# Optimization experiments

Hardware: AMD Instinct MI355X
Metric: run time of the kernel (lower is better)

## Reference

```python
import jax, jax.numpy as jnp
import numpy as np

H = 64; H2 = 32; B = 256; NPART = 64
NP = B * NPART          # 16384 part nodes
PER_TF = 512            # torque/force nodes per graph
NT = B * PER_TF; NF = NT
E = 262144              # edges per edge type
L = 5; T = 4            # 4 main hetero layers + 1 actor layer; 4 edge types
NEG = 0.2; EPS = 1e-5


def _seg_softmax(e, seg, n):
    # softmax over entries sharing the same segment id (along axis 0)
    m = jax.lax.stop_gradient(jax.ops.segment_max(e, seg, num_segments=n))
    ex = jnp.exp(e - m[seg])
    s = jax.ops.segment_sum(ex, seg, num_segments=n)
    return ex / s[seg]


def _gat(x_s, x_d, es, ed, Ws, Wd, a_s, a_d, b, n_dst):
    # PyG GATConv, heads=1, add_self_loops=False, bipartite (x_src, x_dst)
    hs = x_s @ Ws                      # [Ns,H]
    hd = x_d @ Wd                      # [Nd,H]
    e = jax.nn.leaky_relu((hs @ a_s)[es] + (hd @ a_d)[ed], NEG)   # [E]
    al = _seg_softmax(e, ed, n_dst)                                # attn per dst neighborhood
    return jax.ops.segment_sum(al[:, None] * hs[es], ed, num_segments=n_dst) + b


def _hetero_layer(xp, xt, xf, edges, Ws, Wd, a_s, a_d, b):
    # to_hetero(aggr='sum'): one GATConv per edge type, sum into each dst type
    (pts, ptd), (tps, tpd), (pfs, pfd), (fps, fpd) = edges
    out_t = _gat(xp, xt, pts, ptd, Ws[0], Wd[0], a_s[0], a_d[0], b[0], xt.shape[0])
    out_p = (_gat(xt, xp, tps, tpd, Ws[1], Wd[1], a_s[1], a_d[1], b[1], xp.shape[0])
             + _gat(xf, xp, fps, fpd, Ws[3], Wd[3], a_s[3], a_d[3], b[3], xp.shape[0]))
    out_f = _gat(xp, xf, pfs, pfd, Ws[2], Wd[2], a_s[2], a_d[2], b[2], xf.shape[0])
    return out_p, out_t, out_f


def _pool(x):
    # MultiAggregation([max, min, mean]); segments are uniform -> reshape
    xr = x.reshape(B, -1, x.shape[-1])
    return jnp.concatenate([xr.max(1), xr.min(1), xr.mean(1)], axis=-1)


def reference(mass, part_state, torque_x, force_x,
              e_pt_src, e_pt_dst, e_tp_src, e_tp_dst,
              e_pf_src, e_pf_dst, e_fp_src, e_fp_dst,
              batch, part_id,
              emb_parts_W, emb_state, W_src, W_dst, a_src, a_dst, b_conv,
              ln_gamma, ln_beta, out_a_W, out_a_b,
              innet_W, innet_b, full_W, full_b, outnet_W, outnet_b):
    edges = ((e_pt_src, e_pt_dst), (e_tp_src, e_tp_dst),
             (e_pf_src, e_pf_dst), (e_fp_src, e_fp_dst))
    idx = part_state[:, 0] + 2 * part_state[:, 1]
    xp = jnp.concatenate([mass @ emb_parts_W, emb_state[idx]], axis=-1)  # [NP,H]
    xt, xf = torque_x, force_x
    for l in range(4):  # main hetero GAT, ReLU between layers, none after last
        xp, xt, xf = _hetero_layer(xp, xt, xf, edges,
                                   W_src[l], W_dst[l], a_src[l], a_dst[l], b_conv[l])
        if l < 3:
            xp, xt, xf = jax.nn.relu(xp), jax.nn.relu(xt), jax.nn.relu(xf)
    # actor: 1-layer hetero GAT (no activation)
    ap, at, af = _hetero_layer(xp, xt, xf, edges,
                               W_src[4], W_dst[4], a_src[4], a_dst[4], b_conv[4])
    # node LayerNorm
    mu = ap.mean(-1, keepdims=True)
    var = ((ap - mu) ** 2).mean(-1, keepdims=True)
    ra = (ap - mu) / jnp.sqrt(var + EPS) * ln_gamma + ln_beta
    ra = ra @ out_a_W + out_a_b                         # [NP,2]
    soft = _seg_softmax(ra, batch, B)                   # softmax per graph, per channel
    actions = jnp.zeros((B, 2, NPART), dtype=ra.dtype).at[batch, :, part_id].set(soft)
    actions = actions.reshape(B, 2 * NPART)
    rep = jnp.concatenate([_pool(xp), _pool(xt), _pool(xf)], axis=1)   # [B, 9H]
    repV = jax.nn.gelu(rep @ innet_W + innet_b, approximate=False)
    repV = jax.nn.gelu(repV @ full_W + full_b, approximate=False)
    V = jnp.tanh(repV @ outnet_W + outnet_b)            # [B,1]
    return actions, V


def setup_inputs():
    key = jax.random.key(0)
    ks = iter(jax.random.split(key, 40))
    f32 = jnp.float32
    inp = {}
    inp['mass'] = jax.random.uniform(next(ks), (NP, 1), dtype=f32)
    inp['part_state'] = jax.random.randint(next(ks), (NP, 2), 0, 2, dtype=jnp.int32)
    inp['torque_x'] = jax.random.normal(next(ks), (NT, H), dtype=f32)
    inp['force_x'] = jax.random.normal(next(ks), (NF, H), dtype=f32)
    for name, n in [('e_pt_src', NP), ('e_pt_dst', NT), ('e_tp_src', NT), ('e_tp_dst', NP),
                    ('e_pf_src', NP), ('e_pf_dst', NF), ('e_fp_src', NF), ('e_fp_dst', NP)]:
        inp[name] = jax.random.randint(next(ks), (E,), 0, n, dtype=jnp.int32)
    inp['batch'] = (jnp.arange(NP) // NPART).astype(jnp.int32)
    inp['part_id'] = (jnp.arange(NP) % NPART).astype(jnp.int32)
    s = 1.0 / np.sqrt(H)
    inp['emb_parts_W'] = jax.random.normal(next(ks), (1, H2), dtype=f32)
    inp['emb_state'] = jax.random.normal(next(ks), (4, H2), dtype=f32)
    inp['W_src'] = jax.random.normal(next(ks), (L, T, H, H), dtype=f32) * s
    inp['W_dst'] = jax.random.normal(next(ks), (L, T, H, H), dtype=f32) * s
    inp['a_src'] = jax.random.normal(next(ks), (L, T, H), dtype=f32) * s
    inp['a_dst'] = jax.random.normal(next(ks), (L, T, H), dtype=f32) * s
    inp['b_conv'] = jax.random.normal(next(ks), (L, T, H), dtype=f32) * 0.01
    inp['ln_gamma'] = jnp.ones((H,), dtype=f32)
    inp['ln_beta'] = jnp.zeros((H,), dtype=f32)
    inp['out_a_W'] = jax.random.normal(next(ks), (H, 2), dtype=f32) * s
    inp['out_a_b'] = jnp.zeros((2,), dtype=f32)
    inp['innet_W'] = jax.random.normal(next(ks), (9 * H, H), dtype=f32) / np.sqrt(9.0 * H)
    inp['innet_b'] = jnp.zeros((H,), dtype=f32)
    inp['full_W'] = jax.random.normal(next(ks), (H, H), dtype=f32) * s
    inp['full_b'] = jnp.zeros((H,), dtype=f32)
    inp['outnet_W'] = jax.random.normal(next(ks), (H, 1), dtype=f32) * s
    inp['outnet_b'] = jnp.zeros((1,), dtype=f32)
    return inp
```

## Files before the change

### kernel.cpp

```cpp
#include <hip/hip_runtime.h>
#include <math.h>

#define NP_ 16384
#define NT_ 131072
#define NF_ 131072
#define E_  262144
#define B_  256
#define NDTOT 294912
#define E4_  1048576

#define D0 0
#define D1 131072
#define D2 147456
#define D3 278528
#define S0 0
#define S1 16384
#define S2 147456
#define S3 163840

__device__ __forceinline__ float dot4(float4 a, float4 b) {
  return a.x * b.x + a.y * b.y + a.z * b.z + a.w * b.w;
}

__device__ __forceinline__ void gather2(
    int kb0, int ke0, float ad0, const float* __restrict__ aS0, const float* __restrict__ x0,
    int kb1, int ke1, float ad1, const float* __restrict__ aS1, const float* __restrict__ x1,
    const int* __restrict__ sortsrc, int q, int lanebase,
    float4* __restrict__ acc0o, float* __restrict__ si0o,
    float4* __restrict__ acc1o, float* __restrict__ si1o) {
  float4 acc0 = make_float4(0.f, 0.f, 0.f, 0.f);
  float4 acc1 = make_float4(0.f, 0.f, 0.f, 0.f);
  float m0 = -3e38f, m1 = -3e38f, sum0 = 0.f, sum1 = 0.f;
  int len = max(ke0 - kb0, ke1 - kb1);
  for (int c = 0; c < len; c += 16) {
    int k0 = kb0 + c + q, k1 = kb1 + c + q;
    int v0 = k0 < ke0, v1 = k1 < ke1;
    int sx0 = v0 ? sortsrc[k0] : 0;
    int sx1 = v1 ? sortsrc[k1] : 0;
    float e0 = -3e38f, e1 = -3e38f;
    if (v0) { float t = aS0[sx0] + ad0; e0 = t > 0.f ? t : 0.2f * t; }
    if (v1) { float t = aS1[sx1] + ad1; e1 = t > 0.f ? t : 0.2f * t; }
    float cm0 = e0, cm1 = e1;
#pragma unroll
    for (int off = 1; off < 16; off <<= 1) {
      cm0 = fmaxf(cm0, __shfl_xor(cm0, off));
      cm1 = fmaxf(cm1, __shfl_xor(cm1, off));
    }
    float mn0 = fmaxf(m0, cm0), mn1 = fmaxf(m1, cm1);
    float w0 = v0 ? __expf(e0 - mn0) : 0.f;
    float w1 = v1 ? __expf(e1 - mn1) : 0.f;
    float ws0 = w0, ws1 = w1;
#pragma unroll
    for (int off = 1; off < 16; off <<= 1) {
      ws0 += __shfl_xor(ws0, off);
      ws1 += __shfl_xor(ws1, off);
    }
    float r0 = __expf(m0 - mn0), r1 = __expf(m1 - mn1);
    sum0 = sum0 * r0 + ws0;
    sum1 = sum1 * r1 + ws1;
    acc0.x *= r0; acc0.y *= r0; acc0.z *= r0; acc0.w *= r0;
    acc1.x *= r1; acc1.y *= r1; acc1.z *= r1; acc1.w *= r1;
    int cnt0 = ke0 - (kb0 + c); cnt0 = cnt0 < 0 ? 0 : (cnt0 > 16 ? 16 : cnt0);
    int cnt1 = ke1 - (kb1 + c); cnt1 = cnt1 < 0 ? 0 : (cnt1 > 16 ? 16 : cnt1);
    int cmax = max(cnt0, cnt1);
    for (int i = 0; i < cmax; i += 4) {
      float wa0 = __shfl(w0, lanebase + i, 64);
      float wa1 = __shfl(w0, lanebase + i + 1, 64);
      float wa2 = __shfl(w0, lanebase + i + 2, 64);
      float wa3 = __shfl(w0, lanebase + i + 3, 64);
      int sa0 = __shfl(sx0, lanebase + i, 64);
      int sa1 = __shfl(sx0, lanebase + i + 1, 64);
      int sa2 = __shfl(sx0, lanebase + i + 2, 64);
      int sa3 = __shfl(sx0, lanebase + i + 3, 64);
      float wb0 = __shfl(w1, lanebase + i, 64);
      float wb1 = __shfl(w1, lanebase + i + 1, 64);
      float wb2 = __shfl(w1, lanebase + i + 2, 64);
      float wb3 = __shfl(w1, lanebase + i + 3, 64);
      int sb0 = __shfl(sx1, lanebase + i, 64);
      int sb1 = __shfl(sx1, lanebase + i + 1, 64);
      int sb2 = __shfl(sx1, lanebase + i + 2, 64);
      int sb3 = __shfl(sx1, lanebase + i + 3, 64);
      float4 xa0 = *(const float4*)(x0 + (size_t)sa0 * 64 + q * 4);
      float4 xa1 = *(const float4*)(x0 + (size_t)sa1 * 64 + q * 4);
      float4 xa2 = *(const float4*)(x0 + (size_t)sa2 * 64 + q * 4);
      float4 xa3 = *(const float4*)(x0 + (size_t)sa3 * 64 + q * 4);
      float4 xb0 = *(const float4*)(x1 + (size_t)sb0 * 64 + q * 4);
      float4 xb1 = *(const float4*)(x1 + (size_t)sb1 * 64 + q * 4);
      float4 xb2 = *(const float4*)(x1 + (size_t)sb2 * 64 + q * 4);
      float4 xb3 = *(const float4*)(x1 + (size_t)sb3 * 64 + q * 4);
      acc0.x += wa0 * xa0.x + wa1 * xa1.x + wa2 * xa2.x + wa3 * xa3.x;
      acc0.y += wa0 * xa0.y + wa1 * xa1.y + wa2 * xa2.y + wa3 * xa3.y;
      acc0.z += wa0 * xa0.z + wa1 * xa1.z + wa2 * xa2.z + wa3 * xa3.z;
      acc0.w += wa0 * xa0.w + wa1 * xa1.w + wa2 * xa2.w + wa3 * xa3.w;
      acc1.x += wb0 * xb0.x + wb1 * xb1.x + wb2 * xb2.x + wb3 * xb3.x;
      acc1.y += wb0 * xb0.y + wb1 * xb1.y + wb2 * xb2.y + wb3 * xb3.y;
      acc1.z += wb0 * xb0.z + wb1 * xb1.z + wb2 * xb2.z + wb3 * xb3.z;
      acc1.w += wb0 * xb0.w + wb1 * xb1.w + wb2 * xb2.w + wb3 * xb3.w;
    }
    m0 = mn0; m1 = mn1;
  }
  *si0o = (sum0 > 0.f) ? 1.f / sum0 : 0.f;
  *si1o = (sum1 > 0.f) ? 1.f / sum1 : 0.f;
  *acc0o = acc0;
  *acc1o = acc1;
}

__device__ __forceinline__ void gather4(
    int kbA, int keA, float adA,
    int kbB, int keB, float adB,
    int kbC, int keC, float adC,
    int kbD, int keD, float adD,
    const float* __restrict__ aS, const float* __restrict__ x,
    const int* __restrict__ sortsrc, int q, int lanebase,
    float4* accAo, float* siAo, float4* accBo, float* siBo,
    float4* accCo, float* siCo, float4* accDo, float* siDo) {
  float4 aA = make_float4(0.f, 0.f, 0.f, 0.f);
  float4 aB = aA, aC = aA, aDv = aA;
  float mA = -3e38f, mB = -3e38f, mC = -3e38f, mD = -3e38f;
  float sA = 0.f, sB = 0.f, sC = 0.f, sD = 0.f;
  int len = max(max(keA - kbA, keB - kbB), max(keC - kbC, keD - kbD));
  for (int c = 0; c < len; c += 16) {
    int kA = kbA + c + q, kB = kbB + c + q, kC = kbC + c + q, kD = kbD + c + q;
    int vA = kA < keA, vB = kB < keB, vC = kC < keC, vD = kD < keD;
    int iA = vA ? sortsrc[kA] : 0;
    int iB = vB ? sortsrc[kB] : 0;
    int iC = vC ? sortsrc[kC] : 0;
    int iD = vD ? sortsrc[kD] : 0;
    float eA = -3e38f, eB = -3e38f, eC = -3e38f, eD = -3e38f;
    if (vA) { float u = aS[iA] + adA; eA = u > 0.f ? u : 0.2f * u; }
    if (vB) { float u = aS[iB] + adB; eB = u > 0.f ? u : 0.2f * u; }
    if (vC) { float u = aS[iC] + adC; eC = u > 0.f ? u : 0.2f * u; }
    if (vD) { float u = aS[iD] + adD; eD = u > 0.f ? u : 0.2f * u; }
    float cA = eA, cB = eB, cC = eC, cD = eD;
#pragma unroll
    for (int off = 1; off < 16; off <<= 1) {
      cA = fmaxf(cA, __shfl_xor(cA, off));
      cB = fmaxf(cB, __shfl_xor(cB, off));
      cC = fmaxf(cC, __shfl_xor(cC, off));
      cD = fmaxf(cD, __shfl_xor(cD, off));
    }
    float nA = fmaxf(mA, cA), nB = fmaxf(mB, cB);
    float nC = fmaxf(mC, cC), nD = fmaxf(mD, cD);
    float wA = vA ? __expf(eA - nA) : 0.f;
    float wB = vB ? __expf(eB - nB) : 0.f;
    float wC = vC ? __expf(eC - nC) : 0.f;
    float wD = vD ? __expf(eD - nD) : 0.f;
    float uA = wA, uB = wB, uC = wC, uD = wD;
#pragma unroll
    for (int off = 1; off < 16; off <<= 1) {
      uA += __shfl_xor(uA, off);
      uB += __shfl_xor(uB, off);
      uC += __shfl_xor(uC, off);
      uD += __shfl_xor(uD, off);
    }
    float rA = __expf(mA - nA), rB = __expf(mB - nB);
    float rC = __expf(mC - nC), rD = __expf(mD - nD);
    sA = sA * rA + uA; sB = sB * rB + uB;
    sC = sC * rC + uC; sD = sD * rD + uD;
    aA.x *= rA; aA.y *= rA; aA.z *= rA; aA.w *= rA;
    aB.x *= rB; aB.y *= rB; aB.z *= rB; aB.w *= rB;
    aC.x *= rC; aC.y *= rC; aC.z *= rC; aC.w *= rC;
    aDv.x *= rD; aDv.y *= rD; aDv.z *= rD; aDv.w *= rD;
    int dA = keA - (kbA + c); dA = dA < 0 ? 0 : (dA > 16 ? 16 : dA);
    int dB = keB - (kbB + c); dB = dB < 0 ? 0 : (dB > 16 ? 16 : dB);
    int dC = keC - (kbC + c); dC = dC < 0 ? 0 : (dC > 16 ? 16 : dC);
    int dD = keD - (kbD + c); dD = dD < 0 ? 0 : (dD > 16 ? 16 : dD);
    int cmax = max(max(dA, dB), max(dC, dD));
    for (int i = 0; i < cmax; i += 4) {
      {
        float w0 = __shfl(wA, lanebase + i, 64);
        float w1 = __shfl(wA, lanebase + i + 1, 64);
        float w2 = __shfl(wA, lanebase + i + 2, 64);
        float w3 = __shfl(wA, lanebase + i + 3, 64);
        int s0 = __shfl(iA, lanebase + i, 64);
        int s1 = __shfl(iA, lanebase + i + 1, 64);
        int s2 = __shfl(iA, lanebase + i + 2, 64);
        int s3 = __shfl(iA, lanebase + i + 3, 64);
        float4 x0 = *(const float4*)(x + (size_t)s0 * 64 + q * 4);
        float4 x1 = *(const float4*)(x + (size_t)s1 * 64 + q * 4);
        float4 x2 = *(const float4*)(x + (size_t)s2 * 64 + q * 4);
        float4 x3 = *(const float4*)(x + (size_t)s3 * 64 + q * 4);
        aA.x += w0 * x0.x + w1 * x1.x + w2 * x2.x + w3 * x3.x;
        aA.y += w0 * x0.y + w1 * x1.y + w2 * x2.y + w3 * x3.y;
        aA.z += w0 * x0.z + w1 * x1.z + w2 * x2.z + w3 * x3.z;
        aA.w += w0 * x0.w + w1 * x1.w + w2 * x2.w + w3 * x3.w;
      }
      {
        float w0 = __shfl(wB, lanebase + i, 64);
        float w1 = __shfl(wB, lanebase + i + 1, 64);
        float w2 = __shfl(wB, lanebase + i + 2, 64);
        float w3 = __shfl(wB, lanebase + i + 3, 64);
        int s0 = __shfl(iB, lanebase + i, 64);
        int s1 = __shfl(iB, lanebase + i + 1, 64);
        int s2 = __shfl(iB, lanebase + i + 2, 64);
        int s3 = __shfl(iB, lanebase + i + 3, 64);
        float4 x0 = *(const float4*)(x + (size_t)s0 * 64 + q * 4);
        float4 x1 = *(const float4*)(x + (size_t)s1 * 64 + q * 4);
        float4 x2 = *(const float4*)(x + (size_t)s2 * 64 + q * 4);
        float4 x3 = *(const float4*)(x + (size_t)s3 * 64 + q * 4);
        aB.x += w0 * x0.x + w1 * x1.x + w2 * x2.x + w3 * x3.x;
        aB.y += w0 * x0.y + w1 * x1.y + w2 * x2.y + w3 * x3.y;
        aB.z += w0 * x0.z + w1 * x1.z + w2 * x2.z + w3 * x3.z;
        aB.w += w0 * x0.w + w1 * x1.w + w2 * x2.w + w3 * x3.w;
      }
      {
        float w0 = __shfl(wC, lanebase + i, 64);
        float w1 = __shfl(wC, lanebase + i + 1, 64);
        float w2 = __shfl(wC, lanebase + i + 2, 64);
        float w3 = __shfl(wC, lanebase + i + 3, 64);
        int s0 = __shfl(iC, lanebase + i, 64);
        int s1 = __shfl(iC, lanebase + i + 1, 64);
        int s2 = __shfl(iC, lanebase + i + 2, 64);
        int s3 = __shfl(iC, lanebase + i + 3, 64);
        float4 x0 = *(const float4*)(x + (size_t)s0 * 64 + q * 4);
        float4 x1 = *(const float4*)(x + (size_t)s1 * 64 + q * 4);
        float4 x2 = *(const float4*)(x + (size_t)s2 * 64 + q * 4);
        float4 x3 = *(const float4*)(x + (size_t)s3 * 64 + q * 4);
        aC.x += w0 * x0.x + w1 * x1.x + w2 * x2.x + w3 * x3.x;
        aC.y += w0 * x0.y + w1 * x1.y + w2 * x2.y + w3 * x3.y;
        aC.z += w0 * x0.z + w1 * x1.z + w2 * x2.z + w3 * x3.z;
        aC.w += w0 * x0.w + w1 * x1.w + w2 * x2.w + w3 * x3.w;
      }
      {
        float w0 = __shfl(wD, lanebase + i, 64);
        float w1 = __shfl(wD, lanebase + i + 1, 64);
        float w2 = __shfl(wD, lanebase + i + 2, 64);
        float w3 = __shfl(wD, lanebase + i + 3, 64);
        int s0 = __shfl(iD, lanebase + i, 64);
        int s1 = __shfl(iD, lanebase + i + 1, 64);
        int s2 = __shfl(iD, lanebase + i + 2, 64);
        int s3 = __shfl(iD, lanebase + i + 3, 64);
        float4 x0 = *(const float4*)(x + (size_t)s0 * 64 + q * 4);
        float4 x1 = *(const float4*)(x + (size_t)s1 * 64 + q * 4);
        float4 x2 = *(const float4*)(x + (size_t)s2 * 64 + q * 4);
        float4 x3 = *(const float4*)(x + (size_t)s3 * 64 + q * 4);
        aDv.x += w0 * x0.x + w1 * x1.x + w2 * x2.x + w3 * x3.x;
        aDv.y += w0 * x0.y + w1 * x1.y + w2 * x2.y + w3 * x3.y;
        aDv.z += w0 * x0.z + w1 * x1.z + w2 * x2.z + w3 * x3.z;
        aDv.w += w0 * x0.w + w1 * x1.w + w2 * x2.w + w3 * x3.w;
      }
    }
    mA = nA; mB = nB; mC = nC; mD = nD;
  }
  *siAo = (sA > 0.f) ? 1.f / sA : 0.f;
  *siBo = (sB > 0.f) ? 1.f / sB : 0.f;
  *siCo = (sC > 0.f) ? 1.f / sC : 0.f;
  *siDo = (sD > 0.f) ? 1.f / sD : 0.f;
  *accAo = aA; *accBo = aB; *accCo = aC; *accDo = aDv;
}

__global__ void k_wa(const float* __restrict__ Wsrc, const float* __restrict__ Wdst,
                     const float* __restrict__ asrc, const float* __restrict__ adst,
                     float* __restrict__ wsas, float* __restrict__ wdad) {
  int b = blockIdx.x;
  int lt = b >> 1;
  int role = b & 1;
  int k = threadIdx.x;
  const float* W = (role == 0 ? Wsrc : Wdst) + ((size_t)(lt * 64 + k)) * 64;
  const float* a = (role == 0 ? asrc : adst) + lt * 64;
  float s = 0.f;
  for (int i = 0; i < 64; i++) s += W[i] * a[i];
  (role == 0 ? wsas : wdad)[lt * 64 + k] = s;
}

__global__ __launch_bounds__(256) void k_build_xp(const float* __restrict__ mass,
    const int* __restrict__ ps, const float* __restrict__ embW,
    const float* __restrict__ embS, const float* __restrict__ Wsrc,
    const float* __restrict__ wsas, const float* __restrict__ wdad,
    float* __restrict__ hs0, float* __restrict__ hs2,
    float* __restrict__ aS, float* __restrict__ aD) {
  __shared__ float WA[4096], WB[4096];
  int tid = threadIdx.x;
  int n = blockIdx.x * 16 + (tid >> 4);
  int q = tid & 15;
  int lanebase = (tid & 63) & 48;
  {
    const float4* W0g = (const float4*)(Wsrc + (size_t)0 * 4096);
    const float4* W2g = (const float4*)(Wsrc + (size_t)2 * 4096);
#pragma unroll
    for (int i = 0; i < 4; i++) {
      ((float4*)WA)[i * 256 + tid] = W0g[i * 256 + tid];
      ((float4*)WB)[i * 256 + tid] = W2g[i * 256 + tid];
    }
  }
  float4 v;
  if (q < 8) {
    float mv = mass[n];
    const float* e = embW + q * 4;
    v.x = mv * e[0]; v.y = mv * e[1]; v.z = mv * e[2]; v.w = mv * e[3];
  } else {
    int idx = ps[n * 2] + 2 * ps[n * 2 + 1];
    const float4* e = (const float4*)(embS + idx * 32 + (q - 8) * 4);
    v = *e;
  }
  float4 w0 = *(const float4*)(wsas + 0 * 64 + q * 4);
  float4 w2 = *(const float4*)(wsas + 2 * 64 + q * 4);
  float4 d1 = *(const float4*)(wdad + 1 * 64 + q * 4);
  float4 d3 = *(const float4*)(wdad + 3 * 64 + q * 4);
  float p0 = dot4(v, w0), p2 = dot4(v, w2), p1 = dot4(v, d1), p3 = dot4(v, d3);
#pragma unroll
  for (int off = 1; off < 16; off <<= 1) {
    p0 += __shfl_xor(p0, off); p2 += __shfl_xor(p2, off);
    p1 += __shfl_xor(p1, off); p3 += __shfl_xor(p3, off);
  }
  if (q == 0) { aS[S0 + n] = p0; aS[S2 + n] = p2; aD[D1 + n] = p1; aD[D3 + n] = p3; }
  __syncthreads();
  const float4* WAc = (const float4*)WA;
  const float4* WBc = (const float4*)WB;
  float4 h0 = make_float4(0.f, 0.f, 0.f, 0.f);
  float4 h2 = make_float4(0.f, 0.f, 0.f, 0.f);
#pragma unroll 4
  for (int k4 = 0; k4 < 16; k4++) {
    float ax = __shfl(v.x, lanebase + k4, 64);
    float ay = __shfl(v.y, lanebase + k4, 64);
    float az = __shfl(v.z, lanebase + k4, 64);
    float aw = __shfl(v.w, lanebase + k4, 64);
    float4 a0 = WAc[(k4 * 4 + 0) * 16 + q];
    float4 a1 = WAc[(k4 * 4 + 1) * 16 + q];
    float4 a2 = WAc[(k4 * 4 + 2) * 16 + q];
    float4 a3 = WAc[(k4 * 4 + 3) * 16 + q];
    float4 c0 = WBc[(k4 * 4 + 0) * 16 + q];
    float4 c1 = WBc[(k4 * 4 + 1) * 16 + q];
    float4 c2 = WBc[(k4 * 4 + 2) * 16 + q];
    float4 c3 = WBc[(k4 * 4 + 3) * 16 + q];
    h0.x += ax * a0.x + ay * a1.x + az * a2.x + aw * a3.x;
    h0.y += ax * a0.y + ay * a1.y + az * a2.y + aw * a3.y;
    h0.z += ax * a0.z + ay * a1.z + az * a2.z + aw * a3.z;
    h0.w += ax * a0.w + ay * a1.w + az * a2.w + aw * a3.w;
    h2.x += ax * c0.x + ay * c1.x + az * c2.x + aw * c3.x;
    h2.y += ax * c0.y + ay * c1.y + az * c2.y + aw * c3.y;
    h2.z += ax * c0.z + ay * c1.z + az * c2.z + aw * c3.z;
    h2.w += ax * c0.w + ay * c1.w + az * c2.w + aw * c3.w;
  }
  *(float4*)(hs0 + (size_t)n * 64 + q * 4) = h0;
  *(float4*)(hs2 + (size_t)n * 64 + q * 4) = h2;
}

__global__ __launch_bounds__(256) void k_init_dots(const float* __restrict__ tx,
    const float* __restrict__ fx, const float* __restrict__ wsas,
    const float* __restrict__ wdad, float* __restrict__ aS, float* __restrict__ aD) {
  int tid = threadIdx.x;
  int q = tid & 15, slot = tid >> 4;
  int b = blockIdx.x;
  int isF = (b >= 8192);
  int n = (isF ? b - 8192 : b) * 16 + slot;
  const float* src = (isF ? fx : tx) + (size_t)n * 64 + q * 4;
  float4 v = *(const float4*)src;
  int tsrc = isF ? 3 : 1, tdst = isF ? 2 : 0;
  float4 ws = *(const float4*)(wsas + tsrc * 64 + q * 4);
  float4 wd = *(const float4*)(wdad + tdst * 64 + q * 4);
  float pS = dot4(v, ws), pD = dot4(v, wd);
#pragma unroll
  for (int off = 1; off < 16; off <<= 1) {
    pS += __shfl_xor(pS, off); pD += __shfl_xor(pD, off);
  }
  if (q == 0) {
    if (!isF) { aS[S1 + n] = pS; aD[D0 + n] = pD; }
    else      { aS[S3 + n] = pS; aD[D2 + n] = pD; }
  }
}

__global__ __launch_bounds__(256) void k_count(
    const int* __restrict__ d0, const int* __restrict__ d1,
    const int* __restrict__ d2, const int* __restrict__ d3,
    int* __restrict__ counts) {
  __shared__ int cnt[64];
  int b = blockIdx.x;
  int t = b >> 6, c = b & 63;
  const int* dp = (t == 0) ? d0 : (t == 1) ? d1 : (t == 2) ? d2 : d3;
  int sh = (t & 1) ? 8 : 11;
  int tid = threadIdx.x;
  if (tid < 64) cnt[tid] = 0;
  __syncthreads();
  const int4* dp4 = (const int4*)dp + (size_t)c * 1024;
  for (int i = tid; i < 1024; i += 256) {
    int4 v = dp4[i];
    atomicAdd(&cnt[v.x >> sh], 1);
    atomicAdd(&cnt[v.y >> sh], 1);
    atomicAdd(&cnt[v.z >> sh], 1);
    atomicAdd(&cnt[v.w >> sh], 1);
  }
  __syncthreads();
  if (tid < 64) counts[(b << 6) + tid] = cnt[tid];
}

__global__ __launch_bounds__(256) void k_bases(const int* __restrict__ counts,
    int* __restrict__ cbase, int* __restrict__ granBase, int* __restrict__ rowptr) {
  __shared__ int tot[256];
  int tid = threadIdx.x;
  int t = tid >> 6, g = tid & 63;
  int s = 0;
  for (int c = 0; c < 64; c++) s += counts[(((t << 6) | c) << 6) + g];
  tot[tid] = s;
  __syncthreads();
  for (int off = 1; off < 256; off <<= 1) {
    int x = 0; if (tid >= off) x = tot[tid - off];
    __syncthreads(); tot[tid] += x; __syncthreads();
  }
  int gb = tot[tid] - s;
  granBase[tid] = gb;
  if (tid == 255) granBase[256] = E4_;
  if (tid == 0) rowptr[NDTOT] = E4_;
  int run = gb;
  for (int c = 0; c < 64; c++) {
    int idx = (((t << 6) | c) << 6) + g;
    int v = counts[idx];
    cbase[idx] = run;
    run += v;
  }
}

__global__ __launch_bounds__(256) void k_place(
    const int* __restrict__ d0, const int* __restrict__ s0,
    const int* __restrict__ d1, const int* __restrict__ s1,
    const int* __restrict__ d2, const int* __restrict__ s2,
    const int* __restrict__ d3, const int* __restrict__ s3,
    const int* __restrict__ cbase, int2* __restrict__ pairs) {
  __shared__ int cur[64];
  int b = blockIdx.x;
  int t = b >> 6, c = b & 63;
  const int* dp; const int* sp;
  if (t == 0) { dp = d0; sp = s0; }
  else if (t == 1) { dp = d1; sp = s1; }
  else if (t == 2) { dp = d2; sp = s2; }
  else { dp = d3; sp = s3; }
  int sh = (t & 1) ? 8 : 11;
  int tid = threadIdx.x;
  if (tid < 64) cur[tid] = cbase[(b << 6) + tid];
  __syncthreads();
  const int4* dp4 = (const int4*)dp + (size_t)c * 1024;
  const int4* sp4 = (const int4*)sp + (size_t)c * 1024;
  for (int i = tid; i < 1024; i += 256) {
    int4 d = dp4[i];
    int4 s = sp4[i];
    int pos;
    pos = atomicAdd(&cur[d.x >> sh], 1); pairs[pos] = make_int2(d.x, s.x);
    pos = atomicAdd(&cur[d.y >> sh], 1); pairs[pos] = make_int2(d.y, s.y);
    pos = atomicAdd(&cur[d.z >> sh], 1); pairs[pos] = make_int2(d.z, s.z);
    pos = atomicAdd(&cur[d.w >> sh], 1); pairs[pos] = make_int2(d.w, s.w);
  }
}

__global__ __launch_bounds__(256) void k_build(const int2* __restrict__ pairs,
    const int* __restrict__ granBase, int* __restrict__ rowptr,
    int* __restrict__ sortsrc) {
  __shared__ int cnt[2048];
  __shared__ int psum[256];
  int g = blockIdx.x;
  int t = g >> 6, gg = g & 63;
  int rows = (t & 1) ? 256 : 2048;
  int rowLo = gg * rows;
  int csr0;
  if (t == 0) csr0 = D0 + rowLo;
  else if (t == 1) csr0 = D1 + rowLo;
  else if (t == 2) csr0 = D2 + rowLo;
  else csr0 = D3 + rowLo;
  int eb = granBase[g], ee = granBase[g + 1];
  int tid = threadIdx.x;
  for (int i = tid; i < rows; i += 256) cnt[i] = 0;
  __syncthreads();
  for (int i = eb + tid; i < ee; i += 256) {
    int2 p = pairs[i];
    atomicAdd(&cnt[p.x - rowLo], 1);
  }
  __syncthreads();
  int per = rows >> 8;
  int b0 = tid * per;
  int s = 0;
  for (int j = 0; j < per; j++) s += cnt[b0 + j];
  psum[tid] = s;
  __syncthreads();
  for (int off = 1; off < 256; off <<= 1) {
    int x = 0; if (tid >= off) x = psum[tid - off];
    __syncthreads(); psum[tid] += x; __syncthreads();
  }
  int run = psum[tid] - s;
  for (int j = 0; j < per; j++) {
    int v = cnt[b0 + j];
    cnt[b0 + j] = run;
    rowptr[csr0 + b0 + j] = eb + run;
    run += v;
  }
  __syncthreads();
  for (int i = eb + tid; i < ee; i += 256) {
    int2 p = pairs[i];
    int pos = eb + atomicAdd(&cnt[p.x - rowLo], 1);
    sortsrc[pos] = p.y;
  }
}

__global__ __launch_bounds__(256) void k_part(int l,
    const float* __restrict__ Wsrc, const float* __restrict__ bconv,
    const float* __restrict__ xt, const float* __restrict__ xf,
    const int* __restrict__ rowptr, const int* __restrict__ sortsrc,
    const float* __restrict__ aSrd, const float* __restrict__ aDrd,
    float* __restrict__ aSwr, float* __restrict__ aDwr,
    const float* __restrict__ wsas, const float* __restrict__ wdad,
    float* __restrict__ xpo, float* __restrict__ hs0n, float* __restrict__ hs2n,
    int relu, int writeHs, int writeXp,
    const float* __restrict__ gamma, const float* __restrict__ beta,
    const float* __restrict__ oaW, const float* __restrict__ oab,
    float* __restrict__ raOut) {
  __shared__ float WA[4096], WB[4096];
  int tid = threadIdx.x;
  int q = tid & 15;
  int lanebase = (tid & 63) & 48;
  int n = blockIdx.x * 16 + (tid >> 4);
  {
    const float4* W1g = (const float4*)(Wsrc + (size_t)(l * 4 + 1) * 4096);
    const float4* W3g = (const float4*)(Wsrc + (size_t)(l * 4 + 3) * 4096);
#pragma unroll
    for (int i = 0; i < 4; i++) {
      ((float4*)WA)[i * 256 + tid] = W1g[i * 256 + tid];
      ((float4*)WB)[i * 256 + tid] = W3g[i * 256 + tid];
    }
  }
  __syncthreads();

  int row1 = D1 + n, row3 = D3 + n;
  int kb1 = rowptr[row1], ke1 = rowptr[row1 + 1];
  int kb3 = rowptr[row3], ke3 = rowptr[row3 + 1];
  float4 accA, accB; float siA, siB;
  gather2(kb1, ke1, aDrd[row1], aSrd + S1, xt,
          kb3, ke3, aDrd[row3], aSrd + S3, xf,
          sortsrc, q, lanebase, &accA, &siA, &accB, &siB);
  accA.x *= siA; accA.y *= siA; accA.z *= siA; accA.w *= siA;
  accB.x *= siB; accB.y *= siB; accB.z *= siB; accB.w *= siB;

  float4 o;
  {
    float4 b1 = *(const float4*)(bconv + (size_t)(l * 4 + 1) * 64 + q * 4);
    float4 b3 = *(const float4*)(bconv + (size_t)(l * 4 + 3) * 64 + q * 4);
    o = make_float4(b1.x + b3.x, b1.y + b3.y, b1.z + b3.z, b1.w + b3.w);
  }
  const float4* WAc = (const float4*)WA;
  const float4* WBc = (const float4*)WB;
#pragma unroll 4
  for (int k4 = 0; k4 < 16; k4++) {
    float ax = __shfl(accA.x, lanebase + k4, 64);
    float ay = __shfl(accA.y, lanebase + k4, 64);
    float az = __shfl(accA.z, lanebase + k4, 64);
    float aw = __shfl(accA.w, lanebase + k4, 64);
    float bx = __shfl(accB.x, lanebase + k4, 64);
    float by = __shfl(accB.y, lanebase + k4, 64);
    float bz = __shfl(accB.z, lanebase + k4, 64);
    float bw = __shfl(accB.w, lanebase + k4, 64);
    float4 wa0 = WAc[(k4 * 4 + 0) * 16 + q];
    float4 wa1 = WAc[(k4 * 4 + 1) * 16 + q];
    float4 wa2 = WAc[(k4 * 4 + 2) * 16 + q];
    float4 wa3 = WAc[(k4 * 4 + 3) * 16 + q];
    float4 wb0 = WBc[(k4 * 4 + 0) * 16 + q];
    float4 wb1 = WBc[(k4 * 4 + 1) * 16 + q];
    float4 wb2 = WBc[(k4 * 4 + 2) * 16 + q];
    float4 wb3 = WBc[(k4 * 4 + 3) * 16 + q];
    o.x += ax * wa0.x + ay * wa1.x + az * wa2.x + aw * wa3.x
         + bx * wb0.x + by * wb1.x + bz * wb2.x + bw * wb3.x;
    o.y += ax * wa0.y + ay * wa1.y + az * wa2.y + aw * wa3.y
         + bx * wb0.y + by * wb1.y + bz * wb2.y + bw * wb3.y;
    o.z += ax * wa0.z + ay * wa1.z + az * wa2.z + aw * wa3.z
         + bx * wb0.z + by * wb1.z + bz * wb2.z + bw * wb3.z;
    o.w += ax * wa0.w + ay * wa1.w + az * wa2.w + aw * wa3.w
         + bx * wb0.w + by * wb1.w + bz * wb2.w + bw * wb3.w;
  }

  if (raOut) {
    float ssum = o.x + o.y + o.z + o.w;
#pragma unroll
    for (int off = 1; off < 16; off <<= 1) ssum += __shfl_xor(ssum, off);
    float mean = ssum * (1.f / 64.f);
    float dx = o.x - mean, dy = o.y - mean, dz = o.z - mean, dw = o.w - mean;
    float v2 = dx * dx + dy * dy + dz * dz + dw * dw;
#pragma unroll
    for (int off = 1; off < 16; off <<= 1) v2 += __shfl_xor(v2, off);
    float rstd = 1.f / sqrtf(v2 * (1.f / 64.f) + 1e-5f);
    float4 g4 = *(const float4*)(gamma + q * 4);
    float4 be4 = *(const float4*)(beta + q * 4);
    float y0 = dx * rstd * g4.x + be4.x;
    float y1 = dy * rstd * g4.y + be4.y;
    float y2 = dz * rstd * g4.z + be4.z;
    float y3 = dw * rstd * g4.w + be4.w;
    float4 wAv = *(const float4*)(oaW + q * 8);
    float4 wBv = *(const float4*)(oaW + q * 8 + 4);
    float p0 = y0 * wAv.x + y1 * wAv.z + y2 * wBv.x + y3 * wBv.z;
    float p1 = y0 * wAv.y + y1 * wAv.w + y2 * wBv.y + y3 * wBv.w;
#pragma unroll
    for (int off = 1; off < 16; off <<= 1) {
      p0 += __shfl_xor(p0, off);
      p1 += __shfl_xor(p1, off);
    }
    if (q == 0) {
      raOut[(size_t)n * 2]     = p0 + oab[0];
      raOut[(size_t)n * 2 + 1] = p1 + oab[1];
    }
    return;
  }

  if (relu) { o.x = fmaxf(o.x, 0.f); o.y = fmaxf(o.y, 0.f); o.z = fmaxf(o.z, 0.f); o.w = fmaxf(o.w, 0.f); }
  if (writeXp) *(float4*)(xpo + (size_t)n * 64 + q * 4) = o;

  {
    float4 w0 = *(const float4*)(wsas + (size_t)((l + 1) * 4 + 0) * 64 + q * 4);
    float4 w2 = *(const float4*)(wsas + (size_t)((l + 1) * 4 + 2) * 64 + q * 4);
    float4 d1 = *(const float4*)(wdad + (size_t)((l + 1) * 4 + 1) * 64 + q * 4);
    float4 d3 = *(const float4*)(wdad + (size_t)((l + 1) * 4 + 3) * 64 + q * 4);
    float p0 = dot4(o, w0), p2 = dot4(o, w2), p1 = dot4(o, d1), p3 = dot4(o, d3);
#pragma unroll
    for (int off = 1; off < 16; off <<= 1) {
      p0 += __shfl_xor(p0, off); p2 += __shfl_xor(p2, off);
      p1 += __shfl_xor(p1, off); p3 += __shfl_xor(p3, off);
    }
    if (q == 0) { aSwr[S0 + n] = p0; aSwr[S2 + n] = p2; aDwr[D1 + n] = p1; aDwr[D3 + n] = p3; }
  }

  if (writeHs) {
    __syncthreads();
    {
      const float4* W0g = (const float4*)(Wsrc + (size_t)((l + 1) * 4 + 0) * 4096);
      const float4* W2g = (const float4*)(Wsrc + (size_t)((l + 1) * 4 + 2) * 4096);
#pragma unroll
      for (int i = 0; i < 4; i++) {
        ((float4*)WA)[i * 256 + tid] = W0g[i * 256 + tid];
        ((float4*)WB)[i * 256 + tid] = W2g[i * 256 + tid];
      }
    }
    __syncthreads();
    float4 h0 = make_float4(0.f, 0.f, 0.f, 0.f);
    float4 h2 = make_float4(0.f, 0.f, 0.f, 0.f);
#pragma unroll 4
    for (int k4 = 0; k4 < 16; k4++) {
      float ox = __shfl(o.x, lanebase + k4, 64);
      float oy = __shfl(o.y, lanebase + k4, 64);
      float oz = __shfl(o.z, lanebase + k4, 64);
      float ow = __shfl(o.w, lanebase + k4, 64);
      float4 a0 = WAc[(k4 * 4 + 0) * 16 + q];
      float4 a1 = WAc[(k4 * 4 + 1) * 16 + q];
      float4 a2 = WAc[(k4 * 4 + 2) * 16 + q];
      float4 a3 = WAc[(k4 * 4 + 3) * 16 + q];
      float4 c0 = WBc[(k4 * 4 + 0) * 16 + q];
      float4 c1 = WBc[(k4 * 4 + 1) * 16 + q];
      float4 c2 = WBc[(k4 * 4 + 2) * 16 + q];
      float4 c3 = WBc[(k4 * 4 + 3) * 16 + q];
      h0.x += ox * a0.x + oy * a1.x + oz * a2.x + ow * a3.x;
      h0.y += ox * a0.y + oy * a1.y + oz * a2.y + ow * a3.y;
      h0.z += ox * a0.z + oy * a1.z + oz * a2.z + ow * a3.z;
      h0.w += ox * a0.w + oy * a1.w + oz * a2.w + ow * a3.w;
      h2.x += ox * c0.x + oy * c1.x + oz * c2.x + ow * c3.x;
      h2.y += ox * c0.y + oy * c1.y + oz * c2.y + ow * c3.y;
      h2.z += ox * c0.z + oy * c1.z + oz * c2.z + ow * c3.z;
      h2.w += ox * c0.w + oy * c1.w + oz * c2.w + ow * c3.w;
    }
    *(float4*)(hs0n + (size_t)n * 64 + q * 4) = h0;
    *(float4*)(hs2n + (size_t)n * 64 + q * 4) = h2;
  }
}

__global__ __launch_bounds__(256) void k_tf(int l, const float* __restrict__ hs0,
    const float* __restrict__ hs2, const float* __restrict__ bconv,
    const int* __restrict__ rowptr, const int* __restrict__ sortsrc,
    const float* __restrict__ aSrd, const float* __restrict__ aDrd,
    float* __restrict__ aSwr, float* __restrict__ aDwr,
    const float* __restrict__ wsas, const float* __restrict__ wdad,
    float* __restrict__ xt, float* __restrict__ xf, int relu) {
  int tid = threadIdx.x;
  int q = tid & 15, slot = tid >> 4;
  int lanebase = (tid & 63) & 48;
  int b = blockIdx.x;
  int isF = (b >= 2048);
  int r0 = (isF ? b - 2048 : b) * 64 + slot;
  int csr = (isF ? D2 : D0) + r0;
  const float* hs = isF ? hs2 : hs0;
  const float* aSseg = aSrd + (isF ? S2 : S0);
  int t = isF ? 2 : 0;

  int kbA = rowptr[csr],      keA = rowptr[csr + 1];
  int kbB = rowptr[csr + 16], keB = rowptr[csr + 17];
  int kbC = rowptr[csr + 32], keC = rowptr[csr + 33];
  int kbD = rowptr[csr + 48], keD = rowptr[csr + 49];
  float4 aA, aB, aC, aD4; float sA, sB, sC, sD;
  gather4(kbA, keA, aDrd[csr],      kbB, keB, aDrd[csr + 16],
          kbC, keC, aDrd[csr + 32], kbD, keD, aDrd[csr + 48],
          aSseg, hs, sortsrc, q, lanebase,
          &aA, &sA, &aB, &sB, &aC, &sC, &aD4, &sD);

  float4 bias = *(const float4*)(bconv + (size_t)(l * 4 + t) * 64 + q * 4);
  float4 o0, o1, o2, o3;
  o0.x = aA.x * sA + bias.x; o0.y = aA.y * sA + bias.y;
  o0.z = aA.z * sA + bias.z; o0.w = aA.w * sA + bias.w;
  o1.x = aB.x * sB + bias.x; o1.y = aB.y * sB + bias.y;
  o1.z = aB.z * sB + bias.z; o1.w = aB.w * sB + bias.w;
  o2.x = aC.x * sC + bias.x; o2.y = aC.y * sC + bias.y;
  o2.z = aC.z * sC + bias.z; o2.w = aC.w * sC + bias.w;
  o3.x = aD4.x * sD + bias.x; o3.y = aD4.y * sD + bias.y;
  o3.z = aD4.z * sD + bias.z; o3.w = aD4.w * sD + bias.w;
  if (relu) {
    o0.x = fmaxf(o0.x, 0.f); o0.y = fmaxf(o0.y, 0.f); o0.z = fmaxf(o0.z, 0.f); o0.w = fmaxf(o0.w, 0.f);
    o1.x = fmaxf(o1.x, 0.f); o1.y = fmaxf(o1.y, 0.f); o1.z = fmaxf(o1.z, 0.f); o1.w = fmaxf(o1.w, 0.f);
    o2.x = fmaxf(o2.x, 0.f); o2.y = fmaxf(o2.y, 0.f); o2.z = fmaxf(o2.z, 0.f); o2.w = fmaxf(o2.w, 0.f);
    o3.x = fmaxf(o3.x, 0.f); o3.y = fmaxf(o3.y, 0.f); o3.z = fmaxf(o3.z, 0.f); o3.w = fmaxf(o3.w, 0.f);
  }
  float* xout = isF ? xf : xt;
  *(float4*)(xout + (size_t)r0 * 64 + q * 4) = o0;
  *(float4*)(xout + (size_t)(r0 + 16) * 64 + q * 4) = o1;
  *(float4*)(xout + (size_t)(r0 + 32) * 64 + q * 4) = o2;
  *(float4*)(xout + (size_t)(r0 + 48) * 64 + q * 4) = o3;

  int tsrc = isF ? 3 : 1, tdst = isF ? 2 : 0;
  float4 wsv = *(const float4*)(wsas + (size_t)((l + 1) * 4 + tsrc) * 64 + q * 4);
  float4 wdv = *(const float4*)(wdad + (size_t)((l + 1) * 4 + tdst) * 64 + q * 4);
  float pS0 = dot4(o0, wsv), pD0 = dot4(o0, wdv);
  float pS1 = dot4(o1, wsv), pD1 = dot4(o1, wdv);
  float pS2 = dot4(o2, wsv), pD2 = dot4(o2, wdv);
  float pS3 = dot4(o3, wsv), pD3 = dot4(o3, wdv);
#pragma unroll
  for (int off = 1; off < 16; off <<= 1) {
    pS0 += __shfl_xor(pS0, off); pD0 += __shfl_xor(pD0, off);
    pS1 += __shfl_xor(pS1, off); pD1 += __shfl_xor(pD1, off);
    pS2 += __shfl_xor(pS2, off); pD2 += __shfl_xor(pD2, off);
    pS3 += __shfl_xor(pS3, off); pD3 += __shfl_xor(pD3, off);
  }
  if (q == 0) {
    int sb = isF ? S3 : S1;
    int db = isF ? D2 : D0;
    aSwr[sb + r0]      = pS0; aDwr[db + r0]      = pD0;
    aSwr[sb + r0 + 16] = pS1; aDwr[db + r0 + 16] = pD1;
    aSwr[sb + r0 + 32] = pS2; aDwr[db + r0 + 32] = pD2;
    aSwr[sb + r0 + 48] = pS3; aDwr[db + r0 + 48] = pD3;
  }
}

__global__ __launch_bounds__(64) void k_actor(const float* __restrict__ ra,
                                              float* __restrict__ outp) {
  int g = blockIdx.x;
  int p = threadIdx.x;
  float2 rv = *(const float2*)(ra + (size_t)(g * 64 + p) * 2);
  float m0 = rv.x, m1 = rv.y;
  for (int off = 32; off > 0; off >>= 1) {
    m0 = fmaxf(m0, __shfl_xor(m0, off));
    m1 = fmaxf(m1, __shfl_xor(m1, off));
  }
  float e0 = __expf(rv.x - m0), e1 = __expf(rv.y - m1);
  float s0 = e0, s1 = e1;
  for (int off = 32; off > 0; off >>= 1) {
    s0 += __shfl_xor(s0, off);
    s1 += __shfl_xor(s1, off);
  }
  outp[g * 128 + p] = e0 / s0;
  outp[g * 128 + 64 + p] = e1 / s1;
}

__global__ __launch_bounds__(256) void k_pool(const float* __restrict__ xp,
    const float* __restrict__ xt, const float* __restrict__ xf,
    float* __restrict__ pool) {
  __shared__ float pmax[4][64], pmin[4][64], psum[4][64];
  int b = blockIdx.x;
  int g = b / 9, c = b % 9;
  int tid = threadIdx.x;
  int grp = tid >> 6, col = tid & 63;
  const float* src; int R;
  if (c == 0)      { src = xp + (size_t)g * 64 * 64; R = 64; }
  else if (c <= 4) { src = xt + ((size_t)g * 512 + (size_t)(c - 1) * 128) * 64; R = 128; }
  else             { src = xf + ((size_t)g * 512 + (size_t)(c - 5) * 128) * 64; R = 128; }
  float mx = -3e38f, mn = 3e38f, sm = 0.f;
  for (int r = grp; r < R; r += 4) {
    float v = src[(size_t)r * 64 + col];
    mx = fmaxf(mx, v); mn = fminf(mn, v); sm += v;
  }
  pmax[grp][col] = mx; pmin[grp][col] = mn; psum[grp][col] = sm;
  __syncthreads();
  if (grp == 0) {
    float M = fmaxf(fmaxf(pmax[0][col], pmax[1][col]), fmaxf(pmax[2][col], pmax[3][col]));
    float m = fminf(fminf(pmin[0][col], pmin[1][col]), fminf(pmin[2][col], pmin[3][col]));
    float S = psum[0][col] + psum[1][col] + psum[2][col] + psum[3][col];
    float* o = pool + ((size_t)(g * 9 + c) * 3) * 64;
    o[col] = M; o[64 + col] = m; o[128 + col] = S;
  }
}

__global__ __launch_bounds__(256) void k_vhead(const float* __restrict__ pool,
    const float* __restrict__ inW, const float* __restrict__ inb,
    const float* __restrict__ fW, const float* __restrict__ fb,
    const float* __restrict__ oW, const float* __restrict__ ob,
    float* __restrict__ outV) {
  __shared__ float rep[576];
  __shared__ float red[256];
  __shared__ float h1[64];
  int g = blockIdx.x, tid = threadIdx.x;
  if (tid < 64) {
    int col = tid;
    const float* pg = pool + (size_t)g * 9 * 3 * 64;
    rep[col] = pg[col];
    rep[64 + col] = pg[64 + col];
    rep[128 + col] = pg[128 + col] * (1.f / 64.f);
    float M = -3e38f, m = 3e38f, S = 0.f;
    for (int c = 1; c <= 4; c++) {
      const float* p = pg + (size_t)c * 192;
      M = fmaxf(M, p[col]); m = fminf(m, p[64 + col]); S += p[128 + col];
    }
    rep[192 + col] = M; rep[256 + col] = m; rep[320 + col] = S * (1.f / 512.f);
    M = -3e38f; m = 3e38f; S = 0.f;
    for (int c = 5; c <= 8; c++) {
      const float* p = pg + (size_t)c * 192;
      M = fmaxf(M, p[col]); m = fminf(m, p[64 + col]); S += p[128 + col];
    }
    rep[384 + col] = M; rep[448 + col] = m; rep[512 + col] = S * (1.f / 512.f);
  }
  __syncthreads();
  const float ISQ2 = 0.70710678118654752f;
  {
    int j = tid & 63, p = tid >> 6;
    float s = 0.f;
    for (int k = p * 144; k < (p + 1) * 144; k++) s += rep[k] * inW[k * 64 + j];
    red[tid] = s;
  }
  __syncthreads();
  if (tid < 64) {
    float s = red[tid] + red[64 + tid] + red[128 + tid] + red[192 + tid] + inb[tid];
    h1[tid] = 0.5f * s * (1.f + erff(s * ISQ2));
  }
  __syncthreads();
  if (tid < 64) {
    float s = fb[tid];
    for (int k = 0; k < 64; k++) s += h1[k] * fW[k * 64 + tid];
    float h2 = 0.5f * s * (1.f + erff(s * ISQ2));
    float p = h2 * oW[tid];
    for (int off = 32; off > 0; off >>= 1) p += __shfl_xor(p, off);
    if (tid == 0) outV[g] = tanhf(p + ob[0]);
  }
}

extern "C" void kernel_launch(void* const* d_in, const int* in_sizes, int n_in,
                              void* d_out, int out_size, void* d_ws, size_t ws_size,
                              hipStream_t stream) {
  (void)in_sizes; (void)n_in; (void)out_size; (void)ws_size;
  const float* mass = (const float*)d_in[0];
  const int*   ps   = (const int*)d_in[1];
  const float* torque_x = (const float*)d_in[2];
  const float* force_x  = (const float*)d_in[3];
  const int* ept_s = (const int*)d_in[4];  const int* ept_d = (const int*)d_in[5];
  const int* etp_s = (const int*)d_in[6];  const int* etp_d = (const int*)d_in[7];
  const int* epf_s = (const int*)d_in[8];  const int* epf_d = (const int*)d_in[9];
  const int* efp_s = (const int*)d_in[10]; const int* efp_d = (const int*)d_in[11];
  const float* embW  = (const float*)d_in[14];
  const float* embS  = (const float*)d_in[15];
  const float* Wsrc  = (const float*)d_in[16];
  const float* Wdst  = (const float*)d_in[17];
  const float* asrc  = (const float*)d_in[18];
  const float* adst  = (const float*)d_in[19];
  const float* bconv = (const float*)d_in[20];
  const float* gamma = (const float*)d_in[21];
  const float* beta  = (const float*)d_in[22];
  const float* oaW   = (const float*)d_in[23];
  const float* oab   = (const float*)d_in[24];
  const float* inW   = (const float*)d_in[25];
  const float* inb   = (const float*)d_in[26];
  const float* fW    = (const float*)d_in[27];
  const float* fb    = (const float*)d_in[28];
  const float* oW    = (const float*)d_in[29];
  const float* ob    = (const float*)d_in[30];

  char* base = (char*)d_ws;
  size_t off = 0;
  auto alloc = [&](size_t bytes) -> void* {
    void* r = base + off;
    off = (off + bytes + 255) & ~(size_t)255;
    return r;
  };
  float* xp  = (float*)alloc((size_t)NP_ * 64 * 4);
  float* xt  = (float*)alloc((size_t)NT_ * 64 * 4);
  float* xf  = (float*)alloc((size_t)NF_ * 64 * 4);
  float* hs0b[2], *hs2b[2];
  hs0b[0] = (float*)alloc((size_t)NP_ * 64 * 4);
  hs0b[1] = (float*)alloc((size_t)NP_ * 64 * 4);
  hs2b[0] = (float*)alloc((size_t)NP_ * 64 * 4);
  hs2b[1] = (float*)alloc((size_t)NP_ * 64 * 4);
  float* aSb[2], *aDb[2];
  aSb[0] = (float*)alloc((size_t)NDTOT * 4);
  aSb[1] = (float*)alloc((size_t)NDTOT * 4);
  aDb[0] = (float*)alloc((size_t)NDTOT * 4);
  aDb[1] = (float*)alloc((size_t)NDTOT * 4);
  float* wsas = (float*)alloc(1280 * 4);
  float* wdad = (float*)alloc(1280 * 4);
  float* pool = (float*)alloc((size_t)B_ * 9 * 3 * 64 * 4);
  float* ra   = (float*)alloc((size_t)NP_ * 2 * 4);
  int* rowptr = (int*)alloc((size_t)(NDTOT + 1) * 4);
  int* sortsrc = (int*)alloc((size_t)E4_ * 4);
  int2* pairs  = (int2*)alloc((size_t)E4_ * 8);
  int* counts  = (int*)alloc(16384 * 4);
  int* cbase   = (int*)alloc(16384 * 4);
  int* granBase = (int*)alloc(257 * 4);

  k_wa<<<40, 64, 0, stream>>>(Wsrc, Wdst, asrc, adst, wsas, wdad);
  k_build_xp<<<NP_ / 16, 256, 0, stream>>>(mass, ps, embW, embS, Wsrc, wsas, wdad,
                                           hs0b[0], hs2b[0], aSb[0], aDb[0]);
  k_init_dots<<<(NT_ + NF_) / 16, 256, 0, stream>>>(torque_x, force_x,
                                                    wsas, wdad, aSb[0], aDb[0]);
  k_count<<<256, 256, 0, stream>>>(ept_d, etp_d, epf_d, efp_d, counts);
  k_bases<<<1, 256, 0, stream>>>(counts, cbase, granBase, rowptr);
  k_place<<<256, 256, 0, stream>>>(ept_d, ept_s, etp_d, etp_s, epf_d, epf_s,
                                   efp_d, efp_s, cbase, pairs);
  k_build<<<256, 256, 0, stream>>>(pairs, granBase, rowptr, sortsrc);

  for (int l = 0; l < 5; l++) {
    int ri = l & 1, wi = (l + 1) & 1;
    int relu = (l < 3) ? 1 : 0;
    const float* xtr = (l == 0) ? torque_x : xt;
    const float* xfr = (l == 0) ? force_x : xf;
    k_part<<<NP_ / 16, 256, 0, stream>>>(l, Wsrc, bconv, xtr, xfr,
                                         rowptr, sortsrc,
                                         aSb[ri], aDb[ri], aSb[wi], aDb[wi],
                                         wsas, wdad, xp,
                                         hs0b[(l + 1) & 1], hs2b[(l + 1) & 1],
                                         relu, (l < 3) ? 1 : 0, (l == 3) ? 1 : 0,
                                         gamma, beta, oaW, oab,
                                         (l == 4) ? ra : (float*)nullptr);
    if (l < 4)
      k_tf<<<(NT_ + NF_) / 64, 256, 0, stream>>>(l, hs0b[l & 1], hs2b[l & 1], bconv,
                                                 rowptr, sortsrc,
                                                 aSb[ri], aDb[ri], aSb[wi], aDb[wi],
                                                 wsas, wdad, xt, xf, relu);
  }

  float* outp = (float*)d_out;
  k_actor<<<B_, 64, 0, stream>>>(ra, outp);
  k_pool<<<B_ * 9, 256, 0, stream>>>(xp, xt, xf, pool);
  k_vhead<<<B_, 256, 0, stream>>>(pool, inW, inb, fW, fb, oW, ob, outp + B_ * 128);
}
```

Before: 603.6 us.

## Store gathered node features in fp16 and merge part/tf gathers into one launch

Torque/force features and the part-node hs projections are now stored as fp16, halving the bytes moved by the random edge gathers, with accumulation still in fp32. The part-node gather and the torque/force gather are combined into one k_layer kernel whose blocks take either role. The part-node dense transform moves into a separate k_xform kernel that reads gathered aggregates staged in a reused scratch buffer. This trades extra aggregate traffic and fp16 rounding error for less gather bandwidth and better overlap between the part and tf work.

```diff
diff --git a/kernel.cpp b/kernel.cpp
--- a/kernel.cpp
+++ b/kernel.cpp
@@ -1,4 +1,5 @@
 #include <hip/hip_runtime.h>
+#include <hip/hip_fp16.h>
 #include <math.h>
 
 #define NP_ 16384
@@ -18,13 +19,22 @@
 #define S2 147456
 #define S3 163840
 
+typedef _Float16 h4 __attribute__((ext_vector_type(4)));
+
 __device__ __forceinline__ float dot4(float4 a, float4 b) {
   return a.x * b.x + a.y * b.y + a.z * b.z + a.w * b.w;
 }
+__device__ __forceinline__ float4 h4tof4(h4 h) {
+  return make_float4((float)h.x, (float)h.y, (float)h.z, (float)h.w);
+}
+__device__ __forceinline__ h4 f4toh4(float4 f) {
+  h4 h; h.x = (_Float16)f.x; h.y = (_Float16)f.y; h.z = (_Float16)f.z; h.w = (_Float16)f.w;
+  return h;
+}
 
 __device__ __forceinline__ void gather2(
-    int kb0, int ke0, float ad0, const float* __restrict__ aS0, const float* __restrict__ x0,
-    int kb1, int ke1, float ad1, const float* __restrict__ aS1, const float* __restrict__ x1,
+    int kb0, int ke0, float ad0, const float* __restrict__ aS0, const _Float16* __restrict__ x0,
+    int kb1, int ke1, float ad1, const float* __restrict__ aS1, const _Float16* __restrict__ x1,
     const int* __restrict__ sortsrc, int q, int lanebase,
     float4* __restrict__ acc0o, float* __restrict__ si0o,
     float4* __restrict__ acc1o, float* __restrict__ si1o) {
@@ -80,14 +90,14 @@
       int sb1 = __shfl(sx1, lanebase + i + 1, 64);
       int sb2 = __shfl(sx1, lanebase + i + 2, 64);
       int sb3 = __shfl(sx1, lanebase + i + 3, 64);
-      float4 xa0 = *(const float4*)(x0 + (size_t)sa0 * 64 + q * 4);
-      float4 xa1 = *(const float4*)(x0 + (size_t)sa1 * 64 + q * 4);
-      float4 xa2 = *(const float4*)(x0 + (size_t)sa2 * 64 + q * 4);
-      float4 xa3 = *(const float4*)(x0 + (size_t)sa3 * 64 + q * 4);
-      float4 xb0 = *(const float4*)(x1 + (size_t)sb0 * 64 + q * 4);
-      float4 xb1 = *(const float4*)(x1 + (size_t)sb1 * 64 + q * 4);
-      float4 xb2 = *(const float4*)(x1 + (size_t)sb2 * 64 + q * 4);
-      float4 xb3 = *(const float4*)(x1 + (size_t)sb3 * 64 + q * 4);
+      float4 xa0 = h4tof4(*(const h4*)(x0 + (size_t)sa0 * 64 + q * 4));
+      float4 xa1 = h4tof4(*(const h4*)(x0 + (size_t)sa1 * 64 + q * 4));
+      float4 xa2 = h4tof4(*(const h4*)(x0 + (size_t)sa2 * 64 + q * 4));
+      float4 xa3 = h4tof4(*(const h4*)(x0 + (size_t)sa3 * 64 + q * 4));
+      float4 xb0 = h4tof4(*(const h4*)(x1 + (size_t)sb0 * 64 + q * 4));
+      float4 xb1 = h4tof4(*(const h4*)(x1 + (size_t)sb1 * 64 + q * 4));
+      float4 xb2 = h4tof4(*(const h4*)(x1 + (size_t)sb2 * 64 + q * 4));
+      float4 xb3 = h4tof4(*(const h4*)(x1 + (size_t)sb3 * 64 + q * 4));
       acc0.x += wa0 * xa0.x + wa1 * xa1.x + wa2 * xa2.x + wa3 * xa3.x;
       acc0.y += wa0 * xa0.y + wa1 * xa1.y + wa2 * xa2.y + wa3 * xa3.y;
       acc0.z += wa0 * xa0.z + wa1 * xa1.z + wa2 * xa2.z + wa3 * xa3.z;
@@ -110,7 +120,7 @@
     int kbB, int keB, float adB,
     int kbC, int keC, float adC,
     int kbD, int keD, float adD,
-    const float* __restrict__ aS, const float* __restrict__ x,
+    const float* __restrict__ aS, const _Float16* __restrict__ x,
     const int* __restrict__ sortsrc, int q, int lanebase,
     float4* accAo, float* siAo, float4* accBo, float* siBo,
     float4* accCo, float* siCo, float4* accDo, float* siDo) {
@@ -176,10 +186,10 @@
         int s1 = __shfl(iA, lanebase + i + 1, 64);
         int s2 = __shfl(iA, lanebase + i + 2, 64);
         int s3 = __shfl(iA, lanebase + i + 3, 64);
-        float4 x0 = *(const float4*)(x + (size_t)s0 * 64 + q * 4);
-        float4 x1 = *(const float4*)(x + (size_t)s1 * 64 + q * 4);
-        float4 x2 = *(const float4*)(x + (size_t)s2 * 64 + q * 4);
-        float4 x3 = *(const float4*)(x + (size_t)s3 * 64 + q * 4);
+        float4 x0 = h4tof4(*(const h4*)(x + (size_t)s0 * 64 + q * 4));
+        float4 x1 = h4tof4(*(const h4*)(x + (size_t)s1 * 64 + q * 4));
+        float4 x2 = h4tof4(*(const h4*)(x + (size_t)s2 * 64 + q * 4));
+        float4 x3 = h4tof4(*(const h4*)(x + (size_t)s3 * 64 + q * 4));
         aA.x += w0 * x0.x + w1 * x1.x + w2 * x2.x + w3 * x3.x;
         aA.y += w0 * x0.y + w1 * x1.y + w2 * x2.y + w3 * x3.y;
         aA.z += w0 * x0.z + w1 * x1.z + w2 * x2.z + w3 * x3.z;
@@ -194,10 +204,10 @@
         int s1 = __shfl(iB, lanebase + i + 1, 64);
         int s2 = __shfl(iB, lanebase + i + 2, 64);
         int s3 = __shfl(iB, lanebase + i + 3, 64);
-        float4 x0 = *(const float4*)(x + (size_t)s0 * 64 + q * 4);
-        float4 x1 = *(const float4*)(x + (size_t)s1 * 64 + q * 4);
-        float4 x2 = *(const float4*)(x + (size_t)s2 * 64 + q * 4);
-        float4 x3 = *(const float4*)(x + (size_t)s3 * 64 + q * 4);
+        float4 x0 = h4tof4(*(const h4*)(x + (size_t)s0 * 64 + q * 4));
+        float4 x1 = h4tof4(*(const h4*)(x + (size_t)s1 * 64 + q * 4));
+        float4 x2 = h4tof4(*(const h4*)(x + (size_t)s2 * 64 + q * 4));
+        float4 x3 = h4tof4(*(const h4*)(x + (size_t)s3 * 64 + q * 4));
         aB.x += w0 * x0.x + w1 * x1.x + w2 * x2.x + w3 * x3.x;
         aB.y += w0 * x0.y + w1 * x1.y + w2 * x2.y + w3 * x3.y;
         aB.z += w0 * x0.z + w1 * x1.z + w2 * x2.z + w3 * x3.z;
@@ -212,10 +222,10 @@
         int s1 = __shfl(iC, lanebase + i + 1, 64);
         int s2 = __shfl(iC, lanebase + i + 2, 64);
         int s3 = __shfl(iC, lanebase + i + 3, 64);
-        float4 x0 = *(const float4*)(x + (size_t)s0 * 64 + q * 4);
-        float4 x1 = *(const float4*)(x + (size_t)s1 * 64 + q * 4);
-        float4 x2 = *(const float4*)(x + (size_t)s2 * 64 + q * 4);
-        float4 x3 = *(const float4*)(x + (size_t)s3 * 64 + q * 4);
+        float4 x0 = h4tof4(*(const h4*)(x + (size_t)s0 * 64 + q * 4));
+        float4 x1 = h4tof4(*(const h4*)(x + (size_t)s1 * 64 + q * 4));
+        float4 x2 = h4tof4(*(const h4*)(x + (size_t)s2 * 64 + q * 4));
+        float4 x3 = h4tof4(*(const h4*)(x + (size_t)s3 * 64 + q * 4));
         aC.x += w0 * x0.x + w1 * x1.x + w2 * x2.x + w3 * x3.x;
         aC.y += w0 * x0.y + w1 * x1.y + w2 * x2.y + w3 * x3.y;
         aC.z += w0 * x0.z + w1 * x1.z + w2 * x2.z + w3 * x3.z;
@@ -230,10 +240,10 @@
         int s1 = __shfl(iD, lanebase + i + 1, 64);
         int s2 = __shfl(iD, lanebase + i + 2, 64);
         int s3 = __shfl(iD, lanebase + i + 3, 64);
-        float4 x0 = *(const float4*)(x + (size_t)s0 * 64 + q * 4);
-        float4 x1 = *(const float4*)(x + (size_t)s1 * 64 + q * 4);
-        float4 x2 = *(const float4*)(x + (size_t)s2 * 64 + q * 4);
-        float4 x3 = *(const float4*)(x + (size_t)s3 * 64 + q * 4);
+        float4 x0 = h4tof4(*(const h4*)(x + (size_t)s0 * 64 + q * 4));
+        float4 x1 = h4tof4(*(const h4*)(x + (size_t)s1 * 64 + q * 4));
+        float4 x2 = h4tof4(*(const h4*)(x + (size_t)s2 * 64 + q * 4));
+        float4 x3 = h4tof4(*(const h4*)(x + (size_t)s3 * 64 + q * 4));
         aDv.x += w0 * x0.x + w1 * x1.x + w2 * x2.x + w3 * x3.x;
         aDv.y += w0 * x0.y + w1 * x1.y + w2 * x2.y + w3 * x3.y;
         aDv.z += w0 * x0.z + w1 * x1.z + w2 * x2.z + w3 * x3.z;
@@ -267,7 +277,7 @@
     const int* __restrict__ ps, const float* __restrict__ embW,
     const float* __restrict__ embS, const float* __restrict__ Wsrc,
     const float* __restrict__ wsas, const float* __restrict__ wdad,
-    float* __restrict__ hs0, float* __restrict__ hs2,
+    _Float16* __restrict__ hs0, _Float16* __restrict__ hs2,
     float* __restrict__ aS, float* __restrict__ aD) {
   __shared__ float WA[4096], WB[4096];
   int tid = threadIdx.x;
@@ -332,13 +342,14 @@
     h2.z += ax * c0.z + ay * c1.z + az * c2.z + aw * c3.z;
     h2.w += ax * c0.w + ay * c1.w + az * c2.w + aw * c3.w;
   }
-  *(float4*)(hs0 + (size_t)n * 64 + q * 4) = h0;
-  *(float4*)(hs2 + (size_t)n * 64 + q * 4) = h2;
+  *(h4*)(hs0 + (size_t)n * 64 + q * 4) = f4toh4(h0);
+  *(h4*)(hs2 + (size_t)n * 64 + q * 4) = f4toh4(h2);
 }
 
 __global__ __launch_bounds__(256) void k_init_dots(const float* __restrict__ tx,
     const float* __restrict__ fx, const float* __restrict__ wsas,
-    const float* __restrict__ wdad, float* __restrict__ aS, float* __restrict__ aD) {
+    const float* __restrict__ wdad, float* __restrict__ aS, float* __restrict__ aD,
+    _Float16* __restrict__ xth, _Float16* __restrict__ xfh) {
   int tid = threadIdx.x;
   int q = tid & 15, slot = tid >> 4;
   int b = blockIdx.x;
@@ -346,6 +357,7 @@
   int n = (isF ? b - 8192 : b) * 16 + slot;
   const float* src = (isF ? fx : tx) + (size_t)n * 64 + q * 4;
   float4 v = *(const float4*)src;
+  *(h4*)((isF ? xfh : xth) + (size_t)n * 64 + q * 4) = f4toh4(v);
   int tsrc = isF ? 3 : 1, tdst = isF ? 2 : 0;
   float4 ws = *(const float4*)(wsas + tsrc * 64 + q * 4);
   float4 wd = *(const float4*)(wdad + tdst * 64 + q * 4);
@@ -489,14 +501,116 @@
   }
 }
 
-__global__ __launch_bounds__(256) void k_part(int l,
-    const float* __restrict__ Wsrc, const float* __restrict__ bconv,
-    const float* __restrict__ xt, const float* __restrict__ xf,
+__global__ __launch_bounds__(256) void k_layer(int l,
+    const _Float16* __restrict__ xt_old, const _Float16* __restrict__ xf_old,
+    const _Float16* __restrict__ hs0, const _Float16* __restrict__ hs2,
+    const float* __restrict__ bconv,
     const int* __restrict__ rowptr, const int* __restrict__ sortsrc,
     const float* __restrict__ aSrd, const float* __restrict__ aDrd,
     float* __restrict__ aSwr, float* __restrict__ aDwr,
     const float* __restrict__ wsas, const float* __restrict__ wdad,
-    float* __restrict__ xpo, float* __restrict__ hs0n, float* __restrict__ hs2n,
+    float* __restrict__ agg1, float* __restrict__ agg3,
+    _Float16* __restrict__ xt_new, _Float16* __restrict__ xf_new,
+    int relu, int hasTf) {
+  int bid = blockIdx.x;
+  int tid = threadIdx.x;
+  int q = tid & 15;
+  int lanebase = (tid & 63) & 48;
+
+  int isPart, pg = 0, tg = 0;
+  if (!hasTf) { isPart = 1; pg = bid; }
+  else {
+    int g = bid / 5, r = bid - g * 5;
+    if (r == 4) { isPart = 1; pg = g; }
+    else        { isPart = 0; tg = g * 4 + r; }
+  }
+
+  if (isPart) {
+    int n = pg * 16 + (tid >> 4);
+    int row1 = D1 + n, row3 = D3 + n;
+    int kb1 = rowptr[row1], ke1 = rowptr[row1 + 1];
+    int kb3 = rowptr[row3], ke3 = rowptr[row3 + 1];
+    float4 accA, accB; float siA, siB;
+    gather2(kb1, ke1, aDrd[row1], aSrd + S1, xt_old,
+            kb3, ke3, aDrd[row3], aSrd + S3, xf_old,
+            sortsrc, q, lanebase, &accA, &siA, &accB, &siB);
+    accA.x *= siA; accA.y *= siA; accA.z *= siA; accA.w *= siA;
+    accB.x *= siB; accB.y *= siB; accB.z *= siB; accB.w *= siB;
+    *(float4*)(agg1 + (size_t)n * 64 + q * 4) = accA;
+    *(float4*)(agg3 + (size_t)n * 64 + q * 4) = accB;
+    return;
+  }
+
+  int slot = tid >> 4;
+  int isF = (tg >= 2048);
+  int r0 = (isF ? tg - 2048 : tg) * 64 + slot;
+  int csr = (isF ? D2 : D0) + r0;
+  const _Float16* hs = isF ? hs2 : hs0;
+  const float* aSseg = aSrd + (isF ? S2 : S0);
+  int t = isF ? 2 : 0;
+
+  int kbA = rowptr[csr],      keA = rowptr[csr + 1];
+  int kbB = rowptr[csr + 16], keB = rowptr[csr + 17];
+  int kbC = rowptr[csr + 32], keC = rowptr[csr + 33];
+  int kbD = rowptr[csr + 48], keD = rowptr[csr + 49];
+  float4 aA, aB, aC, aD4; float sA, sB, sC, sD;
+  gather4(kbA, keA, aDrd[csr],      kbB, keB, aDrd[csr + 16],
+          kbC, keC, aDrd[csr + 32], kbD, keD, aDrd[csr + 48],
+          aSseg, hs, sortsrc, q, lanebase,
+          &aA, &sA, &aB, &sB, &aC, &sC, &aD4, &sD);
+
+  float4 bias = *(const float4*)(bconv + (size_t)(l * 4 + t) * 64 + q * 4);
+  float4 o0, o1, o2, o3;
+  o0.x = aA.x * sA + bias.x; o0.y = aA.y * sA + bias.y;
+  o0.z = aA.z * sA + bias.z; o0.w = aA.w * sA + bias.w;
+  o1.x = aB.x * sB + bias.x; o1.y = aB.y * sB + bias.y;
+  o1.z = aB.z * sB + bias.z; o1.w = aB.w * sB + bias.w;
+  o2.x = aC.x * sC + bias.x; o2.y = aC.y * sC + bias.y;
+  o2.z = aC.z * sC + bias.z; o2.w = aC.w * sC + bias.w;
+  o3.x = aD4.x * sD + bias.x; o3.y = aD4.y * sD + bias.y;
+  o3.z = aD4.z * sD + bias.z; o3.w = aD4.w * sD + bias.w;
+  if (relu) {
+    o0.x = fmaxf(o0.x, 0.f); o0.y = fmaxf(o0.y, 0.f); o0.z = fmaxf(o0.z, 0.f); o0.w = fmaxf(o0.w, 0.f);
+    o1.x = fmaxf(o1.x, 0.f); o1.y = fmaxf(o1.y, 0.f); o1.z = fmaxf(o1.z, 0.f); o1.w = fmaxf(o1.w, 0.f);
+    o2.x = fmaxf(o2.x, 0.f); o2.y = fmaxf(o2.y, 0.f); o2.z = fmaxf(o2.z, 0.f); o2.w = fmaxf(o2.w, 0.f);
+    o3.x = fmaxf(o3.x, 0.f); o3.y = fmaxf(o3.y, 0.f); o3.z = fmaxf(o3.z, 0.f); o3.w = fmaxf(o3.w, 0.f);
+  }
+  _Float16* xout = isF ? xf_new : xt_new;
+  *(h4*)(xout + (size_t)r0 * 64 + q * 4) = f4toh4(o0);
+  *(h4*)(xout + (size_t)(r0 + 16) * 64 + q * 4) = f4toh4(o1);
+  *(h4*)(xout + (size_t)(r0 + 32) * 64 + q * 4) = f4toh4(o2);
+  *(h4*)(xout + (size_t)(r0 + 48) * 64 + q * 4) = f4toh4(o3);
+
+  int tsrc = isF ? 3 : 1, tdst = isF ? 2 : 0;
+  float4 wsv = *(const float4*)(wsas + (size_t)((l + 1) * 4 + tsrc) * 64 + q * 4);
+  float4 wdv = *(const float4*)(wdad + (size_t)((l + 1) * 4 + tdst) * 64 + q * 4);
+  float pS0 = dot4(o0, wsv), pD0 = dot4(o0, wdv);
+  float pS1 = dot4(o1, wsv), pD1 = dot4(o1, wdv);
+  float pS2 = dot4(o2, wsv), pD2 = dot4(o2, wdv);
+  float pS3 = dot4(o3, wsv), pD3 = dot4(o3, wdv);
+#pragma unroll
+  for (int off = 1; off < 16; off <<= 1) {
+    pS0 += __shfl_xor(pS0, off); pD0 += __shfl_xor(pD0, off);
+    pS1 += __shfl_xor(pS1, off); pD1 += __shfl_xor(pD1, off);
+    pS2 += __shfl_xor(pS2, off); pD2 += __shfl_xor(pD2, off);
+    pS3 += __shfl_xor(pS3, off); pD3 += __shfl_xor(pD3, off);
+  }
+  if (q == 0) {
+    int sb = isF ? S3 : S1;
+    int db = isF ? D2 : D0;
+    aSwr[sb + r0]      = pS0; aDwr[db + r0]      = pD0;
+    aSwr[sb + r0 + 16] = pS1; aDwr[db + r0 + 16] = pD1;
+    aSwr[sb + r0 + 32] = pS2; aDwr[db + r0 + 32] = pD2;
+    aSwr[sb + r0 + 48] = pS3; aDwr[db + r0 + 48] = pD3;
+  }
+}
+
+__global__ __launch_bounds__(256) void k_xform(int l,
+    const float* __restrict__ Wsrc, const float* __restrict__ bconv,
+    const float* __restrict__ agg1, const float* __restrict__ agg3,
+    float* __restrict__ aSwr, float* __restrict__ aDwr,
+    const float* __restrict__ wsas, const float* __restrict__ wdad,
+    float* __restrict__ xpo, _Float16* __restrict__ hs0n, _Float16* __restrict__ hs2n,
     int relu, int writeHs, int writeXp,
     const float* __restrict__ gamma, const float* __restrict__ beta,
     const float* __restrict__ oaW, const float* __restrict__ oab,
@@ -515,17 +629,9 @@
       ((float4*)WB)[i * 256 + tid] = W3g[i * 256 + tid];
     }
   }
-  __syncthreads();
-
-  int row1 = D1 + n, row3 = D3 + n;
-  int kb1 = rowptr[row1], ke1 = rowptr[row1 + 1];
-  int kb3 = rowptr[row3], ke3 = rowptr[row3 + 1];
-  float4 accA, accB; float siA, siB;
-  gather2(kb1, ke1, aDrd[row1], aSrd + S1, xt,
-          kb3, ke3, aDrd[row3], aSrd + S3, xf,
-          sortsrc, q, lanebase, &accA, &siA, &accB, &siB);
-  accA.x *= siA; accA.y *= siA; accA.z *= siA; accA.w *= siA;
-  accB.x *= siB; accB.y *= siB; accB.z *= siB; accB.w *= siB;
+  float4 accA = *(const float4*)(agg1 + (size_t)n * 64 + q * 4);
+  float4 accB = *(const float4*)(agg3 + (size_t)n * 64 + q * 4);
+  __syncthreads();
 
   float4 o;
   {
@@ -649,82 +755,8 @@
       h2.z += ox * c0.z + oy * c1.z + oz * c2.z + ow * c3.z;
       h2.w += ox * c0.w + oy * c1.w + oz * c2.w + ow * c3.w;
     }
-    *(float4*)(hs0n + (size_t)n * 64 + q * 4) = h0;
-    *(float4*)(hs2n + (size_t)n * 64 + q * 4) = h2;
-  }
-}
-
-__global__ __launch_bounds__(256) void k_tf(int l, const float* __restrict__ hs0,
-    const float* __restrict__ hs2, const float* __restrict__ bconv,
-    const int* __restrict__ rowptr, const int* __restrict__ sortsrc,
-    const float* __restrict__ aSrd, const float* __restrict__ aDrd,
-    float* __restrict__ aSwr, float* __restrict__ aDwr,
-    const float* __restrict__ wsas, const float* __restrict__ wdad,
-    float* __restrict__ xt, float* __restrict__ xf, int relu) {
-  int tid = threadIdx.x;
-  int q = tid & 15, slot = tid >> 4;
-  int lanebase = (tid & 63) & 48;
-  int b = blockIdx.x;
-  int isF = (b >= 2048);
-  int r0 = (isF ? b - 2048 : b) * 64 + slot;
-  int csr = (isF ? D2 : D0) + r0;
-  const float* hs = isF ? hs2 : hs0;
-  const float* aSseg = aSrd + (isF ? S2 : S0);
-  int t = isF ? 2 : 0;
-
-  int kbA = rowptr[csr],      keA = rowptr[csr + 1];
-  int kbB = rowptr[csr + 16], keB = rowptr[csr + 17];
-  int kbC = rowptr[csr + 32], keC = rowptr[csr + 33];
-  int kbD = rowptr[csr + 48], keD = rowptr[csr + 49];
-  float4 aA, aB, aC, aD4; float sA, sB, sC, sD;
-  gather4(kbA, keA, aDrd[csr],      kbB, keB, aDrd[csr + 16],
-          kbC, keC, aDrd[csr + 32], kbD, keD, aDrd[csr + 48],
-          aSseg, hs, sortsrc, q, lanebase,
-          &aA, &sA, &aB, &sB, &aC, &sC, &aD4, &sD);
-
-  float4 bias = *(const float4*)(bconv + (size_t)(l * 4 + t) * 64 + q * 4);
-  float4 o0, o1, o2, o3;
-  o0.x = aA.x * sA + bias.x; o0.y = aA.y * sA + bias.y;
-  o0.z = aA.z * sA + bias.z; o0.w = aA.w * sA + bias.w;
-  o1.x = aB.x * sB + bias.x; o1.y = aB.y * sB + bias.y;
-  o1.z = aB.z * sB + bias.z; o1.w = aB.w * sB + bias.w;
-  o2.x = aC.x * sC + bias.x; o2.y = aC.y * sC + bias.y;
-  o2.z = aC.z * sC + bias.z; o2.w = aC.w * sC + bias.w;
-  o3.x = aD4.x * sD + bias.x; o3.y = aD4.y * sD + bias.y;
-  o3.z = aD4.z * sD + bias.z; o3.w = aD4.w * sD + bias.w;
-  if (relu) {
-    o0.x = fmaxf(o0.x, 0.f); o0.y = fmaxf(o0.y, 0.f); o0.z = fmaxf(o0.z, 0.f); o0.w = fmaxf(o0.w, 0.f);
-    o1.x = fmaxf(o1.x, 0.f); o1.y = fmaxf(o1.y, 0.f); o1.z = fmaxf(o1.z, 0.f); o1.w = fmaxf(o1.w, 0.f);
-    o2.x = fmaxf(o2.x, 0.f); o2.y = fmaxf(o2.y, 0.f); o2.z = fmaxf(o2.z, 0.f); o2.w = fmaxf(o2.w, 0.f);
-    o3.x = fmaxf(o3.x, 0.f); o3.y = fmaxf(o3.y, 0.f); o3.z = fmaxf(o3.z, 0.f); o3.w = fmaxf(o3.w, 0.f);
-  }
-  float* xout = isF ? xf : xt;
-  *(float4*)(xout + (size_t)r0 * 64 + q * 4) = o0;
-  *(float4*)(xout + (size_t)(r0 + 16) * 64 + q * 4) = o1;
-  *(float4*)(xout + (size_t)(r0 + 32) * 64 + q * 4) = o2;
-  *(float4*)(xout + (size_t)(r0 + 48) * 64 + q * 4) = o3;
-
-  int tsrc = isF ? 3 : 1, tdst = isF ? 2 : 0;
-  float4 wsv = *(const float4*)(wsas + (size_t)((l + 1) * 4 + tsrc) * 64 + q * 4);
-  float4 wdv = *(const float4*)(wdad + (size_t)((l + 1) * 4 + tdst) * 64 + q * 4);
-  float pS0 = dot4(o0, wsv), pD0 = dot4(o0, wdv);
-  float pS1 = dot4(o1, wsv), pD1 = dot4(o1, wdv);
-  float pS2 = dot4(o2, wsv), pD2 = dot4(o2, wdv);
-  float pS3 = dot4(o3, wsv), pD3 = dot4(o3, wdv);
-#pragma unroll
-  for (int off = 1; off < 16; off <<= 1) {
-    pS0 += __shfl_xor(pS0, off); pD0 += __shfl_xor(pD0, off);
-    pS1 += __shfl_xor(pS1, off); pD1 += __shfl_xor(pD1, off);
-    pS2 += __shfl_xor(pS2, off); pD2 += __shfl_xor(pD2, off);
-    pS3 += __shfl_xor(pS3, off); pD3 += __shfl_xor(pD3, off);
-  }
-  if (q == 0) {
-    int sb = isF ? S3 : S1;
-    int db = isF ? D2 : D0;
-    aSwr[sb + r0]      = pS0; aDwr[db + r0]      = pD0;
-    aSwr[sb + r0 + 16] = pS1; aDwr[db + r0 + 16] = pD1;
-    aSwr[sb + r0 + 32] = pS2; aDwr[db + r0 + 32] = pD2;
-    aSwr[sb + r0 + 48] = pS3; aDwr[db + r0 + 48] = pD3;
+    *(h4*)(hs0n + (size_t)n * 64 + q * 4) = f4toh4(h0);
+    *(h4*)(hs2n + (size_t)n * 64 + q * 4) = f4toh4(h2);
   }
 }
 
@@ -749,21 +781,28 @@
 }
 
 __global__ __launch_bounds__(256) void k_pool(const float* __restrict__ xp,
-    const float* __restrict__ xt, const float* __restrict__ xf,
+    const _Float16* __restrict__ xt, const _Float16* __restrict__ xf,
     float* __restrict__ pool) {
   __shared__ float pmax[4][64], pmin[4][64], psum[4][64];
   int b = blockIdx.x;
   int g = b / 9, c = b % 9;
   int tid = threadIdx.x;
   int grp = tid >> 6, col = tid & 63;
-  const float* src; int R;
-  if (c == 0)      { src = xp + (size_t)g * 64 * 64; R = 64; }
-  else if (c <= 4) { src = xt + ((size_t)g * 512 + (size_t)(c - 1) * 128) * 64; R = 128; }
-  else             { src = xf + ((size_t)g * 512 + (size_t)(c - 5) * 128) * 64; R = 128; }
   float mx = -3e38f, mn = 3e38f, sm = 0.f;
-  for (int r = grp; r < R; r += 4) {
-    float v = src[(size_t)r * 64 + col];
-    mx = fmaxf(mx, v); mn = fminf(mn, v); sm += v;
+  if (c == 0) {
+    const float* src = xp + (size_t)g * 64 * 64;
+    for (int r = grp; r < 64; r += 4) {
+      float v = src[(size_t)r * 64 + col];
+      mx = fmaxf(mx, v); mn = fminf(mn, v); sm += v;
+    }
+  } else {
+    const _Float16* src;
+    if (c <= 4) src = xt + ((size_t)g * 512 + (size_t)(c - 1) * 128) * 64;
+    else        src = xf + ((size_t)g * 512 + (size_t)(c - 5) * 128) * 64;
+    for (int r = grp; r < 128; r += 4) {
+      float v = (float)src[(size_t)r * 64 + col];
+      mx = fmaxf(mx, v); mn = fminf(mn, v); sm += v;
+    }
   }
   pmax[grp][col] = mx; pmin[grp][col] = mn; psum[grp][col] = sm;
   __syncthreads();
@@ -866,13 +905,18 @@
     return r;
   };
   float* xp  = (float*)alloc((size_t)NP_ * 64 * 4);
-  float* xt  = (float*)alloc((size_t)NT_ * 64 * 4);
-  float* xf  = (float*)alloc((size_t)NF_ * 64 * 4);
-  float* hs0b[2], *hs2b[2];
-  hs0b[0] = (float*)alloc((size_t)NP_ * 64 * 4);
-  hs0b[1] = (float*)alloc((size_t)NP_ * 64 * 4);
-  hs2b[0] = (float*)alloc((size_t)NP_ * 64 * 4);
-  hs2b[1] = (float*)alloc((size_t)NP_ * 64 * 4);
+  _Float16* xtb[2]; _Float16* xfb[2];
+  xtb[0] = (_Float16*)alloc((size_t)NT_ * 64 * 2);
+  xtb[1] = (_Float16*)alloc((size_t)NT_ * 64 * 2);
+  xfb[0] = (_Float16*)alloc((size_t)NF_ * 64 * 2);
+  xfb[1] = (_Float16*)alloc((size_t)NF_ * 64 * 2);
+  _Float16* xth = (_Float16*)alloc((size_t)NT_ * 64 * 2);
+  _Float16* xfh = (_Float16*)alloc((size_t)NF_ * 64 * 2);
+  _Float16* hs0b[2]; _Float16* hs2b[2];
+  hs0b[0] = (_Float16*)alloc((size_t)NP_ * 64 * 2);
+  hs0b[1] = (_Float16*)alloc((size_t)NP_ * 64 * 2);
+  hs2b[0] = (_Float16*)alloc((size_t)NP_ * 64 * 2);
+  hs2b[1] = (_Float16*)alloc((size_t)NP_ * 64 * 2);
   float* aSb[2], *aDb[2];
   aSb[0] = (float*)alloc((size_t)NDTOT * 4);
   aSb[1] = (float*)alloc((size_t)NDTOT * 4);
@@ -888,12 +932,15 @@
   int* counts  = (int*)alloc(16384 * 4);
   int* cbase   = (int*)alloc(16384 * 4);
   int* granBase = (int*)alloc(257 * 4);
+  float* agg1 = (float*)pairs;
+  float* agg3 = agg1 + (size_t)NP_ * 64;
 
   k_wa<<<40, 64, 0, stream>>>(Wsrc, Wdst, asrc, adst, wsas, wdad);
   k_build_xp<<<NP_ / 16, 256, 0, stream>>>(mass, ps, embW, embS, Wsrc, wsas, wdad,
                                            hs0b[0], hs2b[0], aSb[0], aDb[0]);
   k_init_dots<<<(NT_ + NF_) / 16, 256, 0, stream>>>(torque_x, force_x,
-                                                    wsas, wdad, aSb[0], aDb[0]);
+                                                    wsas, wdad, aSb[0], aDb[0],
+                                                    xth, xfh);
   k_count<<<256, 256, 0, stream>>>(ept_d, etp_d, epf_d, efp_d, counts);
   k_bases<<<1, 256, 0, stream>>>(counts, cbase, granBase, rowptr);
   k_place<<<256, 256, 0, stream>>>(ept_d, ept_s, etp_d, etp_s, epf_d, epf_s,
@@ -903,25 +950,28 @@
   for (int l = 0; l < 5; l++) {
     int ri = l & 1, wi = (l + 1) & 1;
     int relu = (l < 3) ? 1 : 0;
-    const float* xtr = (l == 0) ? torque_x : xt;
-    const float* xfr = (l == 0) ? force_x : xf;
-    k_part<<<NP_ / 16, 256, 0, stream>>>(l, Wsrc, bconv, xtr, xfr,
-                                         rowptr, sortsrc,
-                                         aSb[ri], aDb[ri], aSb[wi], aDb[wi],
-                                         wsas, wdad, xp,
-                                         hs0b[(l + 1) & 1], hs2b[(l + 1) & 1],
-                                         relu, (l < 3) ? 1 : 0, (l == 3) ? 1 : 0,
-                                         gamma, beta, oaW, oab,
-                                         (l == 4) ? ra : (float*)nullptr);
-    if (l < 4)
-      k_tf<<<(NT_ + NF_) / 64, 256, 0, stream>>>(l, hs0b[l & 1], hs2b[l & 1], bconv,
-                                                 rowptr, sortsrc,
-                                                 aSb[ri], aDb[ri], aSb[wi], aDb[wi],
-                                                 wsas, wdad, xt, xf, relu);
+    const _Float16* xt_old = (l == 0) ? xth : xtb[(l + 1) & 1];
+    const _Float16* xf_old = (l == 0) ? xfh : xfb[(l + 1) & 1];
+    _Float16* xt_new = xtb[l & 1];
+    _Float16* xf_new = xfb[l & 1];
+    int hasTf = (l < 4) ? 1 : 0;
+    int grid = hasTf ? (NP_ / 16 + (NT_ + NF_) / 64) : (NP_ / 16);
+    k_layer<<<grid, 256, 0, stream>>>(l, xt_old, xf_old,
+                                      hs0b[l & 1], hs2b[l & 1], bconv,
+                                      rowptr, sortsrc,
+                                      aSb[ri], aDb[ri], aSb[wi], aDb[wi],
+                                      wsas, wdad, agg1, agg3,
+                                      xt_new, xf_new, relu, hasTf);
+    k_xform<<<NP_ / 16, 256, 0, stream>>>(l, Wsrc, bconv, agg1, agg3,
+                                          aSb[wi], aDb[wi], wsas, wdad,
+                                          xp, hs0b[(l + 1) & 1], hs2b[(l + 1) & 1],
+                                          relu, (l < 3) ? 1 : 0, (l == 3) ? 1 : 0,
+                                          gamma, beta, oaW, oab,
+                                          (l == 4) ? ra : (float*)nullptr);
   }
 
   float* outp = (float*)d_out;
   k_actor<<<B_, 64, 0, stream>>>(ra, outp);
-  k_pool<<<B_ * 9, 256, 0, stream>>>(xp, xt, xf, pool);
+  k_pool<<<B_ * 9, 256, 0, stream>>>(xp, xtb[1], xfb[1], pool);
   k_vhead<<<B_, 256, 0, stream>>>(pool, inW, inb, fW, fb, oW, ob, outp + B_ * 128);
 }
```

After: 550.4 us. 8.8% less time.
